# Optimization experiments

Hardware: AMD Instinct MI355X
Metric: run time of the kernel (lower is better)

The kernel has to match this reference:

```python
import jax, jax.numpy as jnp
import numpy as np

D_MODEL = 1024
NUM_HEADS = 16
D_HEAD = D_MODEL // NUM_HEADS
THETA = 10000.0
B, S = 2, 2048


def setup_inputs() -> dict:
    key = jax.random.key(0)
    ks = jax.random.split(key, 5)
    std = np.sqrt(2.0 / (D_MODEL + D_MODEL))
    x = jax.random.normal(ks[0], (B, S, D_MODEL), dtype=jnp.float32)
    Wq = jax.random.normal(ks[1], (D_MODEL, D_MODEL), dtype=jnp.float32) * std
    Wk = jax.random.normal(ks[2], (D_MODEL, D_MODEL), dtype=jnp.float32) * std
    Wv = jax.random.normal(ks[3], (D_MODEL, D_MODEL), dtype=jnp.float32) * std
    Wo = jax.random.normal(ks[4], (D_MODEL, D_MODEL), dtype=jnp.float32) * std
    token_positions = jnp.arange(S, dtype=jnp.int32)
    return {"x": x, "Wq": Wq, "Wk": Wk, "Wv": Wv, "Wo": Wo,
            "token_positions": token_positions}


def _apply_rope(t, token_positions):
    # t: [B, H, S, d_head]; interleaved (even/odd) RoPE
    dh = t.shape[-1]
    inv_freq = 1.0 / (THETA ** (jnp.arange(0, dh, 2, dtype=jnp.float32) / dh))
    freqs = token_positions.astype(jnp.float32)[:, None] * inv_freq  # [S, dh/2]
    cos = jnp.cos(freqs)  # broadcasts over B, H
    sin = jnp.sin(freqs)
    x1 = t[..., 0::2]
    x2 = t[..., 1::2]
    r1 = x1 * cos - x2 * sin
    r2 = x1 * sin + x2 * cos
    return jnp.stack([r1, r2], axis=-1).reshape(t.shape)


def reference(x, Wq, Wk, Wv, Wo, token_positions):
    b, s, d = x.shape
    h, dh = NUM_HEADS, D_HEAD

    def proj(W):
        y = x @ W.T  # [B, S, D]
        return y.reshape(b, s, h, dh).transpose(0, 2, 1, 3)  # [B, H, S, dh]

    q = _apply_rope(proj(Wq), token_positions)
    k = _apply_rope(proj(Wk), token_positions)
    v = proj(Wv)

    scores = jnp.einsum('bhqd,bhkd->bhqk', q, k) / jnp.sqrt(jnp.float32(dh))
    causal = jnp.tril(jnp.ones((s, s), dtype=bool))
    scores = jnp.where(causal, scores, jnp.float32(-jnp.inf))
    attn = jax.nn.softmax(scores, axis=-1)
    out = jnp.einsum('bhqk,bhkd->bhqd', attn, v)  # [B, H, S, dh]
    out = out.transpose(0, 2, 1, 3).reshape(b, s, d)
    return out @ Wo.T
```

## Files before the change

kernel.cpp:

```cpp
#include <hip/hip_runtime.h>
#include <hip/hip_bf16.h>
#include <math.h>

#define DMODEL 1024
#define NHEAD  16
#define DHEAD  64
#define BATCH  2
#define SEQ    2048
#define MROWS  (BATCH * SEQ)

typedef __attribute__((ext_vector_type(8))) __bf16 bf16x8;
typedef __attribute__((ext_vector_type(4))) float  f32x4;

__device__ __forceinline__ void load16_lds(const ushort* g, ushort* l) {
    __builtin_amdgcn_global_load_lds(
        (const __attribute__((address_space(1))) unsigned int*)g,
        (__attribute__((address_space(3))) unsigned int*)l, 16, 0, 0);
}

__device__ __forceinline__ ushort bf16u(float v) {
    __hip_bfloat16 h = __float2bfloat16(v);
    return *reinterpret_cast<ushort*>(&h);
}

__global__ __launch_bounds__(256)
void cast_all(const float* __restrict__ x,  const float* __restrict__ w0,
              const float* __restrict__ w1, const float* __restrict__ w2,
              const float* __restrict__ w3, ushort* __restrict__ xb,
              ushort* __restrict__ wb) {
    const int idx = (blockIdx.x * 256 + threadIdx.x) * 8;
    const int TEN_ = MROWS * DMODEL;
    const float* src;
    ushort* dst;
    if (idx < TEN_) {
        src = x + idx;  dst = xb + idx;
    } else {
        const int r   = idx - TEN_;
        const int sel = r >> 20;
        const int off = r & (DMODEL * DMODEL - 1);
        src = (sel == 0 ? w0 : sel == 1 ? w1 : sel == 2 ? w2 : w3) + off;
        dst = wb + r;
    }
    const f32x4 a = *reinterpret_cast<const f32x4*>(src);
    const f32x4 b = *reinterpret_cast<const f32x4*>(src + 4);
    bf16x8 o;
    #pragma unroll
    for (int j = 0; j < 4; j++) { o[j] = (__bf16)a[j]; o[4 + j] = (__bf16)b[j]; }
    *reinterpret_cast<bf16x8*>(dst) = o;
}

__global__ __launch_bounds__(256)
void rope_tab(const int* __restrict__ pos, float2* __restrict__ tab) {
    const int idx = blockIdx.x * 256 + threadIdx.x;
    const int s = idx >> 5;
    const int i = idx & 31;
    const float p = (float)pos[s];
    const float inv = exp2f(-(float)i * 0.41524101186092f);
    float sn, cs;
    sincosf(p * inv, &sn, &cs);
    tab[idx] = make_float2(cs, sn);
}

#define QKV_BARRIER() do { asm volatile("" ::: "memory"); \
                           __builtin_amdgcn_s_barrier(); } while (0)

#define RD4(dst, p_)                                                          \
    _Pragma("unroll")                                                         \
    for (int rr_ = 0; rr_ < 4; rr_++)                                         \
        dst[rr_] = *reinterpret_cast<const bf16x8*>((p_) + rr_ * 512);

#define MFMA_G(AFR, BFR, IOFF)                                                \
    __builtin_amdgcn_s_setprio(1);                                            \
    _Pragma("unroll")                                                         \
    for (int im_ = 0; im_ < 4; im_++)                                         \
        _Pragma("unroll")                                                     \
        for (int jn_ = 0; jn_ < 4; jn_++)                                     \
            acc[(IOFF) + im_][jn_] = __builtin_amdgcn_mfma_f32_16x16x32_bf16( \
                AFR[im_], BFR[jn_], acc[(IOFF) + im_][jn_], 0, 0, 0);         \
    __builtin_amdgcn_s_setprio(0);

__global__ __launch_bounds__(512, 2)
void gemm_qkv(const ushort* __restrict__ A, const ushort* __restrict__ B,
              ushort* __restrict__ C, const float2* __restrict__ tab) {
    __shared__ __align__(16) ushort pool[65536];

    const int orig = blockIdx.y * gridDim.x + blockIdx.x;
    const int xcd  = orig & 7;
    const int ixd  = orig >> 3;
    const int by   = xcd * 2 + (ixd / 12);
    const int bx   = ixd % 12;
    const int m0   = by * 256;
    const int n0   = bx * 256;

    const int tid  = threadIdx.x;
    const int lane = tid & 63;
    const int w    = tid >> 6;
    const int l16  = lane & 15;
    const int quad = lane >> 4;
    const int wm   = (w >> 2) * 128;
    const int wn   = (w & 3) * 64;
    const int chq  = (quad ^ ((l16 & 3) ^ ((l16 & 4) >> 1))) << 3;
    const int srow = tid >> 2;
    const int ssc  = (tid & 3) ^ ((srow & 3) ^ ((srow & 4) >> 1));

    const ushort* gA = A + (size_t)(m0 + srow) * DMODEL + ssc * 8;
    const ushort* gB = B + (size_t)(n0 + srow) * DMODEL + ssc * 8;

    auto stageA = [&](int tt, int ks) {
        const int off = tt * 64 + ks * 32;
        const int lb  = ((tt & 1) << 15) + (ks << 13);
        load16_lds(gA + off,                &pool[lb + tid * 8]);
        load16_lds(gA + 128 * DMODEL + off, &pool[lb + 4096 + tid * 8]);
    };
    auto stageB = [&](int tt, int ks) {
        const int off = tt * 64 + ks * 32;
        const int lb  = ((tt & 1) << 15) + 16384 + (ks << 13);
        load16_lds(gB + off,                &pool[lb + tid * 8]);
        load16_lds(gB + 128 * DMODEL + off, &pool[lb + 4096 + tid * 8]);
    };

    stageA(0, 0); stageB(0, 0);
    stageA(0, 1); stageB(0, 1);
    stageA(1, 0); stageB(1, 0);

    f32x4 acc[8][4];
    #pragma unroll
    for (int i = 0; i < 8; i++)
        #pragma unroll
        for (int j = 0; j < 4; j++) acc[i][j] = (f32x4){0.f, 0.f, 0.f, 0.f};

    asm volatile("s_waitcnt vmcnt(4)" ::: "memory");
    __builtin_amdgcn_s_barrier();

    bf16x8 al[4], ah[4], bc[4], bn[4];

    { const ushort* p = pool + (wm + l16) * 32 + chq;           RD4(al, p); }
    { const ushort* q = pool + 16384 + (wn + l16) * 32 + chq;   RD4(bc, q); }

    #pragma unroll 1
    for (int t = 0; t < 16; t++) {
        const int buf  = (t & 1) << 15;
        const int bufn = buf ^ 32768;
        if (t <= 14) { stageA(t + 1, 1); stageB(t + 1, 1); }
        { const ushort* p = pool + buf + (wm + 64 + l16) * 32 + chq;
          RD4(ah, p); }
        MFMA_G(al, bc, 0);
        { const ushort* p = pool + buf + 8192 + (wm + l16) * 32 + chq;
          RD4(al, p);
          const ushort* q = pool + buf + 16384 + 8192 + (wn + l16) * 32 + chq;
          RD4(bn, q); }
        MFMA_G(ah, bc, 4);
        if (t <= 14) { asm volatile("s_waitcnt vmcnt(4)" ::: "memory"); }
        QKV_BARRIER();
        if (t <= 13) { stageA(t + 2, 0); stageB(t + 2, 0); }
        { const ushort* p = pool + buf + 8192 + (wm + 64 + l16) * 32 + chq;
          RD4(ah, p); }
        MFMA_G(al, bn, 0);
        if (t <= 14) {
            const ushort* p = pool + bufn + (wm + l16) * 32 + chq;
            RD4(al, p);
            const ushort* q = pool + bufn + 16384 + (wn + l16) * 32 + chq;
            RD4(bc, q);
        }
        MFMA_G(ah, bn, 4);
        if (t <= 13)      { asm volatile("s_waitcnt vmcnt(4)" ::: "memory"); }
        else if (t == 14) { asm volatile("s_waitcnt vmcnt(0)" ::: "memory"); }
        QKV_BARRIER();
    }

    const int nbase  = n0 + wn;
    const int tensor = nbase >> 10;
    const int hh     = (nbase & 1023) >> 6;
    if (tensor < 2) {
        ushort* Dt = C + (size_t)tensor * ((size_t)MROWS * DMODEL);
        #pragma unroll
        for (int i = 0; i < 8; i++)
            #pragma unroll
            for (int r = 0; r < 4; r++) {
                const int m  = m0 + wm + i * 16 + quad * 4 + r;
                const int bb = m >> 11;
                const int ss = m & (SEQ - 1);
                const float2* trow = tab + ss * 32;
                #pragma unroll
                for (int j = 0; j < 4; j++) {
                    const int f = j * 16 + l16;
                    const float2 cs = trow[f >> 1];
                    const float val = acc[i][j][r];
                    const float prt = __shfl_xor(val, 1, 64);
                    const float out = (f & 1) ? (prt * cs.y + val * cs.x)
                                              : (val * cs.x - prt * cs.y);
                    Dt[(((size_t)(bb * NHEAD + hh)) * SEQ + ss) * DHEAD + f] =
                        bf16u(out);
                }
            }
    } else {
        ushort* Tw = pool + w * 8192;
        #pragma unroll
        for (int i = 0; i < 8; i++)
            #pragma unroll
            for (int j = 0; j < 4; j++) {
                const int f  = j * 16 + l16;
                const int sx = (f & 7) << 3;
                #pragma unroll
                for (int r = 0; r < 4; r += 2) {
                    const int ml = i * 16 + quad * 4 + r;
                    ushort2 pk;
                    pk.x = bf16u(acc[i][j][r]);
                    pk.y = bf16u(acc[i][j][r + 1]);
                    *reinterpret_cast<ushort2*>(&Tw[f * 128 + (ml ^ sx)]) = pk;
                }
            }
        asm volatile("s_waitcnt lgkmcnt(0)" ::: "memory");
        ushort* Dv = C + 2 * ((size_t)MROWS * DMODEL);
        const int c  = lane & 15;
        const int fb = lane >> 4;
        #pragma unroll
        for (int rr = 0; rr < 16; rr++) {
            const int fl = rr * 4 + fb;
            const uint4 v = *reinterpret_cast<const uint4*>(
                &Tw[fl * 128 + ((c << 3) ^ ((fl & 7) << 3))]);
            *reinterpret_cast<uint4*>(
                &Dv[(size_t)(hh * 64 + fl) * MROWS + m0 + wm + (c << 3)]) = v;
        }
    }
}

#define RD2(dst, p_)                                                          \
    _Pragma("unroll")                                                         \
    for (int rr_ = 0; rr_ < 2; rr_++)                                         \
        dst[rr_] = *reinterpret_cast<const bf16x8*>((p_) + rr_ * 512);

#define OUT_MFMA_G(AFR, BFR, IOFF)                                            \
    __builtin_amdgcn_s_setprio(1);                                            \
    _Pragma("unroll")                                                         \
    for (int im_ = 0; im_ < 2; im_++)                                         \
        _Pragma("unroll")                                                     \
        for (int jn_ = 0; jn_ < 2; jn_++)                                     \
            acc[(IOFF) + im_][jn_] = __builtin_amdgcn_mfma_f32_16x16x32_bf16( \
                AFR[im_], BFR[jn_], acc[(IOFF) + im_][jn_], 0, 0, 0);         \
    __builtin_amdgcn_s_setprio(0);

__global__ __launch_bounds__(512, 2)
void gemm_out128(const ushort* __restrict__ A, const ushort* __restrict__ B,
                 float* __restrict__ C) {
    __shared__ __align__(16) ushort pool[32768];

    const int orig = blockIdx.y * gridDim.x + blockIdx.x;
    const int n0   = (orig & 7) * 128;
    const int m0   = (orig >> 3) * 128;

    const int tid  = threadIdx.x;
    const int lane = tid & 63;
    const int w    = tid >> 6;
    const int l16  = lane & 15;
    const int quad = lane >> 4;
    const int wm   = (w >> 2) * 64;
    const int wn   = (w & 3) * 32;
    const int chq  = (quad ^ ((l16 & 3) ^ ((l16 & 4) >> 1))) << 3;
    const int srow = tid >> 2;
    const int ssc  = (tid & 3) ^ ((srow & 3) ^ ((srow & 4) >> 1));

    const int am  = m0 + srow;
    const int abb = am >> 11;
    const int ass = am & (SEQ - 1);
    const ushort* gA = A + ((size_t)(abb * NHEAD)) * SEQ * DHEAD
                         + (size_t)ass * DHEAD + ssc * 8;
    const ushort* gB = B + (size_t)(n0 + srow) * DMODEL + ssc * 8;

    auto stageA = [&](int tt, int ks) {
        load16_lds(gA + tt * (SEQ * DHEAD) + ks * 32,
                   &pool[((tt & 1) << 14) + (ks << 12) + tid * 8]);
    };
    auto stageB = [&](int tt, int ks) {
        load16_lds(gB + tt * 64 + ks * 32,
                   &pool[((tt & 1) << 14) + 8192 + (ks << 12) + tid * 8]);
    };

    stageA(0, 0); stageB(0, 0);
    stageA(0, 1); stageB(0, 1);
    stageA(1, 0); stageB(1, 0);

    f32x4 acc[4][2];
    #pragma unroll
    for (int i = 0; i < 4; i++)
        #pragma unroll
        for (int j = 0; j < 2; j++) acc[i][j] = (f32x4){0.f, 0.f, 0.f, 0.f};

    asm volatile("s_waitcnt vmcnt(2)" ::: "memory");
    __builtin_amdgcn_s_barrier();

    bf16x8 al[2], ah[2], bc[2], bn[2];

    { const ushort* p = pool + (wm + l16) * 32 + chq;          RD2(al, p); }
    { const ushort* q = pool + 8192 + (wn + l16) * 32 + chq;   RD2(bc, q); }

    #pragma unroll 1
    for (int t = 0; t < 16; t++) {
        const int buf  = (t & 1) << 14;
        const int bufn = buf ^ 16384;
        if (t <= 14) { stageA(t + 1, 1); stageB(t + 1, 1); }
        { const ushort* p = pool + buf + (wm + 32 + l16) * 32 + chq;
          RD2(ah, p); }
        OUT_MFMA_G(al, bc, 0);
        { const ushort* p = pool + buf + 4096 + (wm + l16) * 32 + chq;
          RD2(al, p);
          const ushort* q = pool + buf + 8192 + 4096 + (wn + l16) * 32 + chq;
          RD2(bn, q); }
        OUT_MFMA_G(ah, bc, 2);
        if (t <= 14) { asm volatile("s_waitcnt vmcnt(2)" ::: "memory"); }
        QKV_BARRIER();
        if (t <= 13) { stageA(t + 2, 0); stageB(t + 2, 0); }
        { const ushort* p = pool + buf + 4096 + (wm + 32 + l16) * 32 + chq;
          RD2(ah, p); }
        OUT_MFMA_G(al, bn, 0);
        if (t <= 14) {
            const ushort* p = pool + bufn + (wm + l16) * 32 + chq;
            RD2(al, p);
            const ushort* q = pool + bufn + 8192 + (wn + l16) * 32 + chq;
            RD2(bc, q);
        }
        OUT_MFMA_G(ah, bn, 2);
        if (t <= 13)      { asm volatile("s_waitcnt vmcnt(2)" ::: "memory"); }
        else if (t == 14) { asm volatile("s_waitcnt vmcnt(0)" ::: "memory"); }
        QKV_BARRIER();
    }

    #pragma unroll
    for (int i = 0; i < 4; i++)
        #pragma unroll
        for (int r = 0; r < 4; r++) {
            const int m = m0 + wm + i * 16 + quad * 4 + r;
            #pragma unroll
            for (int j = 0; j < 2; j++)
                C[(size_t)m * DMODEL + n0 + wn + j * 16 + l16] = acc[i][j][r];
        }
}

__global__ __launch_bounds__(256)
void attn_mfma6(const ushort* __restrict__ qb, const ushort* __restrict__ kb,
                const ushort* __restrict__ vtg, ushort* __restrict__ ob) {
    __shared__ __align__(16) ushort Ks[2][4096];
    __shared__ __align__(16) ushort Vs[2][4096];
    __shared__ ushort Pb[4][16][72];

    const int bh   = blockIdx.x;
    const int b    = bh >> 4;
    const int h    = bh & 15;
    const int qt   = (gridDim.y - 1) - blockIdx.y;
    const int tid  = threadIdx.x;
    const int w    = tid >> 6;
    const int lane = tid & 63;
    const int l16  = lane & 15;
    const int quad = lane >> 4;
    const size_t base = (size_t)bh * SEQ * DHEAD;

    const int qlo = qt * 64 + w * 16;

    const float SC = 0.125f * 1.44269504088896f;
    bf16x8 qa[2];
    {
        const size_t qo = base + (size_t)(qlo + l16) * DHEAD + quad * 8;
        qa[0] = *reinterpret_cast<const bf16x8*>(qb + qo);
        qa[1] = *reinterpret_cast<const bf16x8*>(qb + qo + 32);
        #pragma unroll
        for (int j = 0; j < 8; j++) {
            qa[0][j] = (__bf16)(SC * (float)qa[0][j]);
            qa[1][j] = (__bf16)(SC * (float)qa[1][j]);
        }
    }

    f32x4 oacc[4];
    #pragma unroll
    for (int s = 0; s < 4; s++) oacc[s] = (f32x4){0.f, 0.f, 0.f, 0.f};
    float l_ = 0.f;

    const int c0 = tid,        r0 = c0 >> 3, g0 = (c0 & 7) ^ (r0 & 7);
    const int c1 = 256 + tid,  r1 = c1 >> 3, g1 = (c1 & 7) ^ (r1 & 7);
    const ushort* kg0 = kb + base + (size_t)r0 * DHEAD + g0 * 8;
    const ushort* kg1 = kb + base + (size_t)r1 * DHEAD + g1 * 8;
    const ushort* vg0 = vtg + (size_t)(h * DHEAD + r0) * MROWS + b * SEQ + g0 * 8;
    const ushort* vg1 = vtg + (size_t)(h * DHEAD + r1) * MROWS + b * SEQ + g1 * 8;

    int koff[2][4];
    #pragma unroll
    for (int half = 0; half < 2; half++)
        #pragma unroll
        for (int sub = 0; sub < 4; sub++)
            koff[half][sub] = (sub * 16 + l16) * 64 +
                              (((half * 4 + quad) ^ (l16 & 7)) * 8);

    load16_lds(kg0, &Ks[0][c0 * 8]);
    load16_lds(kg1, &Ks[0][c1 * 8]);
    load16_lds(vg0, &Vs[0][c0 * 8]);
    load16_lds(vg1, &Vs[0][c1 * 8]);

    const int T = qt + 1;
    for (int t = 0; t < T; t++) {
        const int bf = t & 1;
        __syncthreads();
        if (t + 1 < T) {
            const size_t ko = (size_t)(t + 1) * 64 * DHEAD;
            const int    vo = (t + 1) * 64;
            load16_lds(kg0 + ko, &Ks[bf ^ 1][c0 * 8]);
            load16_lds(kg1 + ko, &Ks[bf ^ 1][c1 * 8]);
            load16_lds(vg0 + vo, &Vs[bf ^ 1][c0 * 8]);
            load16_lds(vg1 + vo, &Vs[bf ^ 1][c1 * 8]);
        }

        const bool diag = (t == qt);
        const int nsub = diag ? (w + 1) : 4;
        const int nhv  = diag ? ((w >> 1) + 1) : 2;

        f32x4 sacc[4];
        #pragma unroll
        for (int s = 0; s < 4; s++) sacc[s] = (f32x4){0.f, 0.f, 0.f, 0.f};
        #pragma unroll
        for (int half = 0; half < 2; half++)
            #pragma unroll
            for (int sub = 0; sub < 4; sub++)
                if (sub < nsub) {
                    const bf16x8 kf = *reinterpret_cast<const bf16x8*>(
                        &Ks[bf][koff[half][sub]]);
                    sacc[sub] = __builtin_amdgcn_mfma_f32_16x16x32_bf16(
                        kf, qa[half], sacc[sub], 0, 0, 0);
                }

        float ev[4][4];
        if (diag) {
            const int thr = qlo + l16 - t * 64;
            #pragma unroll
            for (int sub = 0; sub < 4; sub++)
                #pragma unroll
                for (int r = 0; r < 4; r++) {
                    const float e = (sub * 16 + quad * 4 + r <= thr)
                                        ? exp2f(sacc[sub][r]) : 0.f;
                    ev[sub][r] = e;
                    l_ += e;
                }
        } else {
            #pragma unroll
            for (int sub = 0; sub < 4; sub++)
                #pragma unroll
                for (int r = 0; r < 4; r++) {
                    const float e = exp2f(sacc[sub][r]);
                    ev[sub][r] = e;
                    l_ += e;
                }
        }

        #pragma unroll
        for (int sub = 0; sub < 4; sub++) {
            ushort4 pk;
            pk.x = bf16u(ev[sub][0]); pk.y = bf16u(ev[sub][1]);
            pk.z = bf16u(ev[sub][2]); pk.w = bf16u(ev[sub][3]);
            *reinterpret_cast<ushort4*>(&Pb[w][l16][sub * 16 + quad * 4]) = pk;
        }
        bf16x8 pa[2];
        pa[0] = *reinterpret_cast<const bf16x8*>(&Pb[w][l16][quad * 8]);
        pa[1] = *reinterpret_cast<const bf16x8*>(&Pb[w][l16][32 + quad * 8]);

        #pragma unroll
        for (int hk = 0; hk < 2; hk++) {
            if (hk >= nhv) break;
            #pragma unroll
            for (int sf = 0; sf < 4; sf++) {
                const bf16x8 vf = *reinterpret_cast<const bf16x8*>(
                    &Vs[bf][koff[hk][sf]]);
                oacc[sf] = __builtin_amdgcn_mfma_f32_16x16x32_bf16(
                    pa[hk], vf, oacc[sf], 0, 0, 0);
            }
        }
    }

    l_ += __shfl_xor(l_, 16, 64);
    l_ += __shfl_xor(l_, 32, 64);
    float inv[4];
    #pragma unroll
    for (int r = 0; r < 4; r++) inv[r] = 1.f / __shfl(l_, quad * 4 + r, 64);
    #pragma unroll
    for (int sub = 0; sub < 4; sub++)
        #pragma unroll
        for (int r = 0; r < 4; r++) {
            const int q = qlo + quad * 4 + r;
            ob[base + (size_t)q * DHEAD + sub * 16 + l16] =
                bf16u(oacc[sub][r] * inv[r]);
        }
}

extern "C" void kernel_launch(void* const* d_in, const int* in_sizes, int n_in,
                              void* d_out, int out_size, void* d_ws, size_t ws_size,
                              hipStream_t stream) {
    const float* x  = (const float*)d_in[0];
    const float* Wq = (const float*)d_in[1];
    const float* Wk = (const float*)d_in[2];
    const float* Wv = (const float*)d_in[3];
    const float* Wo = (const float*)d_in[4];
    const int* pos = (const int*)d_in[5];

    const size_t TEN = (size_t)MROWS * DMODEL;
    const size_t WEL = (size_t)DMODEL * DMODEL;
    ushort* xb   = (ushort*)d_ws;
    ushort* Wqkv = xb + TEN;
    ushort* Wob  = Wqkv + 3 * WEL;
    ushort* qb   = Wob + WEL;
    ushort* kb   = qb + TEN;
    ushort* vtb  = kb + TEN;
    ushort* ob   = vtb + TEN;
    float2* tab  = (float2*)(ob + TEN);

    dim3 blk(256);
    rope_tab<<<(SEQ * 32) / 256, blk, 0, stream>>>(pos, tab);
    cast_all<<<(TEN + 4 * WEL) / (8 * 256), blk, 0, stream>>>(
        x, Wq, Wk, Wv, Wo, xb, Wqkv);

    dim3 gqkv(3 * DMODEL / 256, MROWS / 256);
    gemm_qkv<<<gqkv, dim3(512), 0, stream>>>(xb, Wqkv, qb, tab);

    dim3 gattn(BATCH * NHEAD, SEQ / 64);
    attn_mfma6<<<gattn, blk, 0, stream>>>(qb, kb, vtb, ob);

    dim3 gout(DMODEL / 128, MROWS / 128);
    gemm_out128<<<gout, dim3(512), 0, stream>>>(ob, Wob, (float*)d_out);
}
```

Measured before the change: 177.9 us.

## Load V fragments directly from global into registers and merge prep kernels

The attention kernel stops staging V tiles through double-buffered shared memory and instead has each lane load its MFMA B-operand fragments straight from the transposed V in global memory at the start of each tile. This halves the LDS footprint and removes the V LDS read traffic, at the cost of uncoalesced-ish global loads whose latency must be hidden by the QK and softmax work. The row-sum accumulator is split into four partial sums to shorten the dependency chain. The cast and RoPE-table kernels are fused into one launch to save a kernel launch.

```diff
diff --git a/kernel.cpp b/kernel.cpp
--- a/kernel.cpp
+++ b/kernel.cpp
@@ -24,41 +24,42 @@
 }
 
 __global__ __launch_bounds__(256)
-void cast_all(const float* __restrict__ x,  const float* __restrict__ w0,
+void prep_all(const float* __restrict__ x,  const float* __restrict__ w0,
               const float* __restrict__ w1, const float* __restrict__ w2,
-              const float* __restrict__ w3, ushort* __restrict__ xb,
-              ushort* __restrict__ wb) {
-    const int idx = (blockIdx.x * 256 + threadIdx.x) * 8;
-    const int TEN_ = MROWS * DMODEL;
-    const float* src;
-    ushort* dst;
-    if (idx < TEN_) {
-        src = x + idx;  dst = xb + idx;
+              const float* __restrict__ w3, const int* __restrict__ pos,
+              ushort* __restrict__ xb, ushort* __restrict__ wb,
+              float2* __restrict__ tab) {
+    const int bid = blockIdx.x;
+    if (bid < 4096) {
+        const int idx = (bid * 256 + threadIdx.x) * 8;
+        const int TEN_ = MROWS * DMODEL;
+        const float* src;
+        ushort* dst;
+        if (idx < TEN_) {
+            src = x + idx;  dst = xb + idx;
+        } else {
+            const int r   = idx - TEN_;
+            const int sel = r >> 20;
+            const int off = r & (DMODEL * DMODEL - 1);
+            src = (sel == 0 ? w0 : sel == 1 ? w1 : sel == 2 ? w2 : w3) + off;
+            dst = wb + r;
+        }
+        const f32x4 a = *reinterpret_cast<const f32x4*>(src);
+        const f32x4 b = *reinterpret_cast<const f32x4*>(src + 4);
+        bf16x8 o;
+        #pragma unroll
+        for (int j = 0; j < 4; j++) { o[j] = (__bf16)a[j]; o[4 + j] = (__bf16)b[j]; }
+        *reinterpret_cast<bf16x8*>(dst) = o;
     } else {
-        const int r   = idx - TEN_;
-        const int sel = r >> 20;
-        const int off = r & (DMODEL * DMODEL - 1);
-        src = (sel == 0 ? w0 : sel == 1 ? w1 : sel == 2 ? w2 : w3) + off;
-        dst = wb + r;
+        const int idx = (bid - 4096) * 256 + threadIdx.x;
+        const int s = idx >> 5;
+        const int i = idx & 31;
+        const float p = (float)pos[s];
+        const float inv = exp2f(-(float)i * 0.41524101186092f);
+        float sn, cs;
+        sincosf(p * inv, &sn, &cs);
+        tab[idx] = make_float2(cs, sn);
     }
-    const f32x4 a = *reinterpret_cast<const f32x4*>(src);
-    const f32x4 b = *reinterpret_cast<const f32x4*>(src + 4);
-    bf16x8 o;
-    #pragma unroll
-    for (int j = 0; j < 4; j++) { o[j] = (__bf16)a[j]; o[4 + j] = (__bf16)b[j]; }
-    *reinterpret_cast<bf16x8*>(dst) = o;
-}
-
-__global__ __launch_bounds__(256)
-void rope_tab(const int* __restrict__ pos, float2* __restrict__ tab) {
-    const int idx = blockIdx.x * 256 + threadIdx.x;
-    const int s = idx >> 5;
-    const int i = idx & 31;
-    const float p = (float)pos[s];
-    const float inv = exp2f(-(float)i * 0.41524101186092f);
-    float sn, cs;
-    sincosf(p * inv, &sn, &cs);
-    tab[idx] = make_float2(cs, sn);
 }
 
 #define QKV_BARRIER() do { asm volatile("" ::: "memory"); \
@@ -337,10 +338,9 @@
 }
 
 __global__ __launch_bounds__(256)
-void attn_mfma6(const ushort* __restrict__ qb, const ushort* __restrict__ kb,
+void attn_mfma9(const ushort* __restrict__ qb, const ushort* __restrict__ kb,
                 const ushort* __restrict__ vtg, ushort* __restrict__ ob) {
     __shared__ __align__(16) ushort Ks[2][4096];
-    __shared__ __align__(16) ushort Vs[2][4096];
     __shared__ ushort Pb[4][16][72];
 
     const int bh   = blockIdx.x;
@@ -372,14 +372,15 @@
     f32x4 oacc[4];
     #pragma unroll
     for (int s = 0; s < 4; s++) oacc[s] = (f32x4){0.f, 0.f, 0.f, 0.f};
-    float l_ = 0.f;
+    f32x4 l4 = (f32x4){0.f, 0.f, 0.f, 0.f};
 
     const int c0 = tid,        r0 = c0 >> 3, g0 = (c0 & 7) ^ (r0 & 7);
     const int c1 = 256 + tid,  r1 = c1 >> 3, g1 = (c1 & 7) ^ (r1 & 7);
     const ushort* kg0 = kb + base + (size_t)r0 * DHEAD + g0 * 8;
     const ushort* kg1 = kb + base + (size_t)r1 * DHEAD + g1 * 8;
-    const ushort* vg0 = vtg + (size_t)(h * DHEAD + r0) * MROWS + b * SEQ + g0 * 8;
-    const ushort* vg1 = vtg + (size_t)(h * DHEAD + r1) * MROWS + b * SEQ + g1 * 8;
+
+    const ushort* vB = vtg + (size_t)(h * DHEAD + l16) * MROWS + b * SEQ
+                           + quad * 8;
 
     int koff[2][4];
     #pragma unroll
@@ -391,20 +392,22 @@
 
     load16_lds(kg0, &Ks[0][c0 * 8]);
     load16_lds(kg1, &Ks[0][c1 * 8]);
-    load16_lds(vg0, &Vs[0][c0 * 8]);
-    load16_lds(vg1, &Vs[0][c1 * 8]);
 
     const int T = qt + 1;
     for (int t = 0; t < T; t++) {
         const int bf = t & 1;
         __syncthreads();
+        bf16x8 vr[2][4];
+        #pragma unroll
+        for (int hk = 0; hk < 2; hk++)
+            #pragma unroll
+            for (int sf = 0; sf < 4; sf++)
+                vr[hk][sf] = *reinterpret_cast<const bf16x8*>(
+                    vB + (size_t)(sf * 16) * MROWS + t * 64 + hk * 32);
         if (t + 1 < T) {
             const size_t ko = (size_t)(t + 1) * 64 * DHEAD;
-            const int    vo = (t + 1) * 64;
             load16_lds(kg0 + ko, &Ks[bf ^ 1][c0 * 8]);
             load16_lds(kg1 + ko, &Ks[bf ^ 1][c1 * 8]);
-            load16_lds(vg0 + vo, &Vs[bf ^ 1][c0 * 8]);
-            load16_lds(vg1 + vo, &Vs[bf ^ 1][c1 * 8]);
         }
 
         const bool diag = (t == qt);
@@ -435,7 +438,7 @@
                     const float e = (sub * 16 + quad * 4 + r <= thr)
                                         ? exp2f(sacc[sub][r]) : 0.f;
                     ev[sub][r] = e;
-                    l_ += e;
+                    l4[sub] += e;
                 }
         } else {
             #pragma unroll
@@ -444,7 +447,7 @@
                 for (int r = 0; r < 4; r++) {
                     const float e = exp2f(sacc[sub][r]);
                     ev[sub][r] = e;
-                    l_ += e;
+                    l4[sub] += e;
                 }
         }
 
@@ -463,15 +466,13 @@
         for (int hk = 0; hk < 2; hk++) {
             if (hk >= nhv) break;
             #pragma unroll
-            for (int sf = 0; sf < 4; sf++) {
-                const bf16x8 vf = *reinterpret_cast<const bf16x8*>(
-                    &Vs[bf][koff[hk][sf]]);
+            for (int sf = 0; sf < 4; sf++)
                 oacc[sf] = __builtin_amdgcn_mfma_f32_16x16x32_bf16(
-                    pa[hk], vf, oacc[sf], 0, 0, 0);
-            }
+                    pa[hk], vr[hk][sf], oacc[sf], 0, 0, 0);
         }
     }
 
+    float l_ = (l4[0] + l4[1]) + (l4[2] + l4[3]);
     l_ += __shfl_xor(l_, 16, 64);
     l_ += __shfl_xor(l_, 32, 64);
     float inv[4];
@@ -509,15 +510,14 @@
     float2* tab  = (float2*)(ob + TEN);
 
     dim3 blk(256);
-    rope_tab<<<(SEQ * 32) / 256, blk, 0, stream>>>(pos, tab);
-    cast_all<<<(TEN + 4 * WEL) / (8 * 256), blk, 0, stream>>>(
-        x, Wq, Wk, Wv, Wo, xb, Wqkv);
+    prep_all<<<4096 + 256, blk, 0, stream>>>(x, Wq, Wk, Wv, Wo, pos,
+                                             xb, Wqkv, tab);
 
     dim3 gqkv(3 * DMODEL / 256, MROWS / 256);
     gemm_qkv<<<gqkv, dim3(512), 0, stream>>>(xb, Wqkv, qb, tab);
 
     dim3 gattn(BATCH * NHEAD, SEQ / 64);
-    attn_mfma6<<<gattn, blk, 0, stream>>>(qb, kb, vtb, ob);
+    attn_mfma9<<<gattn, blk, 0, stream>>>(qb, kb, vtb, ob);
 
     dim3 gout(DMODEL / 128, MROWS / 128);
     gemm_out128<<<gout, dim3(512), 0, stream>>>(ob, Wob, (float*)d_out);
```

Result: slower. 209.2 us (+17.6%).
